# Optimization experiments

Measured on AMD Instinct MI355X. Metric: run time of the kernel, lower is better.

## Reference

```python
import jax, jax.numpy as jnp
import numpy as np

D_MODEL = 1024
N_HEADS = 16
HEAD_DIM = 64  # 16*64 = 1024
LATENT = 256   # low-rank KV compression dim
NUM_WHEELS = 4
WHEEL_OUT = 256


def setup_inputs() -> dict:
    key = jax.random.key(0)
    ks = jax.random.split(key, 9)
    S = 2048
    s = lambda fan_in: 1.0 / np.sqrt(fan_in)
    return {
        "sketch_emb": jax.random.normal(ks[0], (S, D_MODEL), dtype=jnp.float32),
        "Wq": jax.random.normal(ks[1], (D_MODEL, N_HEADS * HEAD_DIM), dtype=jnp.float32) * s(D_MODEL),
        "Wdkv": jax.random.normal(ks[2], (D_MODEL, LATENT), dtype=jnp.float32) * s(D_MODEL),
        "Wuk": jax.random.normal(ks[3], (LATENT, N_HEADS * HEAD_DIM), dtype=jnp.float32) * s(LATENT),
        "Wuv": jax.random.normal(ks[4], (LATENT, N_HEADS * HEAD_DIM), dtype=jnp.float32) * s(LATENT),
        "Wo": jax.random.normal(ks[5], (N_HEADS * HEAD_DIM, D_MODEL), dtype=jnp.float32) * s(N_HEADS * HEAD_DIM),
        "wheel_W": jax.random.normal(ks[6], (NUM_WHEELS, D_MODEL, WHEEL_OUT), dtype=jnp.float32) * s(D_MODEL),
        "wheel_b": jax.random.normal(ks[7], (NUM_WHEELS, WHEEL_OUT), dtype=jnp.float32) * 0.01,
    }


def reference(sketch_emb, Wq, Wdkv, Wuk, Wuv, Wo, wheel_W, wheel_b):
    S = sketch_emb.shape[0]
    # Multi-head latent attention: per-head Q, shared low-rank KV latent.
    q = (sketch_emb @ Wq).reshape(S, N_HEADS, HEAD_DIM)          # [S,H,D]
    c_kv = sketch_emb @ Wdkv                                      # [S,L]
    k = (c_kv @ Wuk).reshape(S, N_HEADS, HEAD_DIM)                # [S,H,D]
    v = (c_kv @ Wuv).reshape(S, N_HEADS, HEAD_DIM)                # [S,H,D]
    scale = 1.0 / np.sqrt(HEAD_DIM).astype(np.float32)
    scores = jnp.einsum("qhd,khd->hqk", q, k) * scale             # [H,S,S]
    attn = jax.nn.softmax(scores, axis=-1)
    ctx = jnp.einsum("hqk,khd->qhd", attn, v).reshape(S, N_HEADS * HEAD_DIM)
    body = ctx @ Wo                                               # [S,1024]
    # Wheel projections batched as one einsum, then laid out as concat order
    # cat([body, w0, w1, w2, w3], dim=1)
    wheels = jnp.einsum("sd,wde->swe", body, wheel_W) + wheel_b   # [S,W,256]
    wheels = wheels.reshape(S, NUM_WHEELS * WHEEL_OUT)
    return jnp.concatenate([body, wheels], axis=1)                # [S,2048]
```

## Files before the change

kernel.cpp:

```cpp
#include <hip/hip_runtime.h>
#include <math.h>

#define S_LEN 2048
#define DMODEL 1024
#define NHEADS 16
#define HDIM 64
#define QPITCH 1280

typedef _Float16 f16x8 __attribute__((ext_vector_type(8)));
typedef _Float16 f16x4 __attribute__((ext_vector_type(4)));
typedef float    f32x4 __attribute__((ext_vector_type(4)));

__device__ __forceinline__ void gld_lds16(void* lds, const void* g) {
    __builtin_amdgcn_global_load_lds(
        (__attribute__((address_space(1))) void*)(g),
        (__attribute__((address_space(3))) void*)(lds), 16, 0, 0);
}

__device__ __forceinline__ void gemm_core(
    _Float16* sA, _Float16* sB,
    const _Float16* __restrict__ A, int lda,
    const _Float16* __restrict__ Bt, int ldb,
    int nkt,
    _Float16* __restrict__ Cb, int ldcb, int bmode,
    _Float16* __restrict__ Cb2, int ldcb2,
    int bx, int by)
{
    const int tid  = threadIdx.x;
    const int lane = tid & 63;
    const int w    = tid >> 6;
    const int quad = lane >> 4;
    const int c0   = lane & 15;
    const int m0 = by * 128;
    const int n0 = bx * 128;

    const int srow = lane >> 3;
    const int sc   = lane & 7;
    const _Float16* a_src[4]; const _Float16* b_src[4];
    int dstoff[4];
#pragma unroll
    for (int t = 0; t < 4; t++) {
        const int row = w * 32 + t * 8 + srow;
        const int c = sc ^ (row & 7);
        a_src[t] = A  + (size_t)(m0 + row) * lda + c * 8;
        b_src[t] = Bt + (size_t)(n0 + row) * ldb + c * 8;
        dstoff[t] = (w * 32 + t * 8) * 64;
    }

    const int mw = (w & 1) * 64;
    const int nw = (w >> 1) * 64;
    int arow[4], brow[4];
#pragma unroll
    for (int i = 0; i < 4; i++) {
        arow[i] = mw + i * 16 + c0;
        brow[i] = nw + i * 16 + c0;
    }

    f32x4 acc[4][4];
#pragma unroll
    for (int i = 0; i < 4; i++)
#pragma unroll
        for (int j = 0; j < 4; j++) acc[i][j] = (f32x4){0.f, 0.f, 0.f, 0.f};

    auto stage = [&](int buf) {
#pragma unroll
        for (int t = 0; t < 4; t++) {
            gld_lds16(&sA[buf * 8192 + dstoff[t]], a_src[t]); a_src[t] += 64;
            gld_lds16(&sB[buf * 8192 + dstoff[t]], b_src[t]); b_src[t] += 64;
        }
    };
    auto step = [&](int buf) {
#pragma unroll
        for (int ks = 0; ks < 2; ks++) {
            const int cb = ks * 4 + quad;
            f16x8 af[4], bfv[4];
#pragma unroll
            for (int i = 0; i < 4; i++)
                af[i] = *(const f16x8*)&sA[buf * 8192 + arow[i] * 64 + ((cb ^ (arow[i] & 7)) << 3)];
#pragma unroll
            for (int j = 0; j < 4; j++)
                bfv[j] = *(const f16x8*)&sB[buf * 8192 + brow[j] * 64 + ((cb ^ (brow[j] & 7)) << 3)];
#pragma unroll
            for (int i = 0; i < 4; i++)
#pragma unroll
                for (int j = 0; j < 4; j++)
                    acc[i][j] = __builtin_amdgcn_mfma_f32_16x16x32_f16(af[i], bfv[j], acc[i][j], 0, 0, 0);
        }
    };

    stage(0);
    for (int kt = 0; kt < nkt; kt += 2) {
        __syncthreads();
        stage(1);
        step(0);
        __syncthreads();
        if (kt + 2 < nkt) stage(0);
        step(1);
    }

#pragma unroll
    for (int i = 0; i < 4; i++) {
#pragma unroll
        for (int reg = 0; reg < 4; reg++) {
            const int m = m0 + mw + i * 16 + quad * 4 + reg;
#pragma unroll
            for (int j = 0; j < 4; j++) {
                const int n = n0 + nw + j * 16 + c0;
                _Float16 hv = (_Float16)acc[i][j][reg];
                if (bmode == 0) {
                    Cb[(size_t)m * ldcb + n] = hv;
                } else {
                    if (n < 1024) Cb[(size_t)m * ldcb + n] = hv;
                    else {
                        const int col = (m & ~63) | (((m & 15) << 2) | ((m >> 4) & 3));
                        Cb2[(size_t)(n - 1024) * ldcb2 + col] = hv;
                    }
                }
            }
        }
    }
}

__global__ __launch_bounds__(256) void gemm_qcwf(
    const _Float16* __restrict__ WcT, const _Float16* __restrict__ Wo_f16,
    _Float16* __restrict__ BtWheels,
    const _Float16* __restrict__ emb_f16, const _Float16* __restrict__ Wqc_t,
    _Float16* __restrict__ qc_f16)
{
    __shared__ _Float16 sA[2][8192];
    __shared__ _Float16 sB[2][8192];
    int b = blockIdx.x;
    if (b < 64) {
        gemm_core(&sA[0][0], &sB[0][0], WcT, 1024, Wo_f16, 1024, 16,
                  BtWheels, 1024, 0, nullptr, 0, b >> 3, b & 7);
    } else {
        b -= 64;
        gemm_core(&sA[0][0], &sB[0][0], emb_f16, 1024, Wqc_t, 1024, 16,
                  qc_f16, 1280, 0, nullptr, 0, b >> 4, b & 15);
    }
}

__global__ __launch_bounds__(256) void gemm_kv(
    const _Float16* __restrict__ qc_f16, const _Float16* __restrict__ Wukv_t,
    _Float16* __restrict__ k_f16, _Float16* __restrict__ vT_f16)
{
    __shared__ _Float16 sA[2][8192];
    __shared__ _Float16 sB[2][8192];
    const int b = blockIdx.x;
    gemm_core(&sA[0][0], &sB[0][0], qc_f16 + 1024, 1280, Wukv_t, 256, 4,
              k_f16, 1024, 4, vT_f16, 2048, b >> 4, b & 15);
}

__global__ __launch_bounds__(256) void gemm_fin64(
    const _Float16* __restrict__ A,
    const _Float16* __restrict__ Bt,
    float* __restrict__ out,
    const float* __restrict__ bias)
{
    __shared__ _Float16 sA[2][64 * 64];
    __shared__ _Float16 sB[2][128 * 64];

    const int tid  = threadIdx.x;
    const int lane = tid & 63;
    const int w    = tid >> 6;
    const int quad = lane >> 4;
    const int c0   = lane & 15;

    const int flat = blockIdx.x;
    const int xcd  = flat & 7;
    const int wi   = flat >> 3;
    const int by   = (xcd & 3) * 8 + (wi & 7);
    const int bx   = (xcd >> 2) * 8 + (wi >> 3);
    const int m0 = by * 64;
    const int n0 = bx * 128;

    const int srow = lane >> 3;
    const int sc   = lane & 7;
    const _Float16* a_src[2]; int a_dst[2];
#pragma unroll
    for (int t = 0; t < 2; t++) {
        const int row = t * 32 + w * 8 + srow;
        const int c = sc ^ (row & 7);
        a_src[t] = A + (size_t)(m0 + row) * 1024 + c * 8;
        a_dst[t] = (t * 32 + w * 8) * 64;
    }
    const _Float16* b_src[4]; int b_dst[4];
#pragma unroll
    for (int t = 0; t < 4; t++) {
        const int row = t * 32 + w * 8 + srow;
        const int c = sc ^ (row & 7);
        b_src[t] = Bt + (size_t)(n0 + row) * 1024 + c * 8;
        b_dst[t] = (t * 32 + w * 8) * 64;
    }

    const int mw = (w & 1) * 32;
    const int nw = (w >> 1) * 64;
    int arow[2], brow[4];
#pragma unroll
    for (int i = 0; i < 2; i++) arow[i] = mw + i * 16 + c0;
#pragma unroll
    for (int j = 0; j < 4; j++) brow[j] = nw + j * 16 + c0;

    f32x4 acc[2][4];
#pragma unroll
    for (int i = 0; i < 2; i++)
#pragma unroll
        for (int j = 0; j < 4; j++) acc[i][j] = (f32x4){0.f, 0.f, 0.f, 0.f};

    auto stage = [&](int buf) {
#pragma unroll
        for (int t = 0; t < 2; t++) { gld_lds16(&sA[buf][a_dst[t]], a_src[t]); a_src[t] += 64; }
#pragma unroll
        for (int t = 0; t < 4; t++) { gld_lds16(&sB[buf][b_dst[t]], b_src[t]); b_src[t] += 64; }
    };
    auto step = [&](int buf) {
#pragma unroll
        for (int ks = 0; ks < 2; ks++) {
            const int cb = ks * 4 + quad;
            f16x8 af[2], bfv[4];
#pragma unroll
            for (int i = 0; i < 2; i++)
                af[i] = *(const f16x8*)&sA[buf][arow[i] * 64 + ((cb ^ (arow[i] & 7)) << 3)];
#pragma unroll
            for (int j = 0; j < 4; j++)
                bfv[j] = *(const f16x8*)&sB[buf][brow[j] * 64 + ((cb ^ (brow[j] & 7)) << 3)];
#pragma unroll
            for (int i = 0; i < 2; i++)
#pragma unroll
                for (int j = 0; j < 4; j++)
                    acc[i][j] = __builtin_amdgcn_mfma_f32_16x16x32_f16(af[i], bfv[j], acc[i][j], 0, 0, 0);
        }
    };

    stage(0);
    for (int kt = 0; kt < 16; kt += 2) {
        __syncthreads();
        stage(1);
        step(0);
        __syncthreads();
        if (kt + 2 < 16) stage(0);
        step(1);
    }

    float bias_v[4];
#pragma unroll
    for (int j = 0; j < 4; j++) bias_v[j] = bias[n0 + nw + j * 16 + c0];
#pragma unroll
    for (int i = 0; i < 2; i++) {
#pragma unroll
        for (int reg = 0; reg < 4; reg++) {
            const int m = m0 + mw + i * 16 + quad * 4 + reg;
#pragma unroll
            for (int j = 0; j < 4; j++) {
                const int n = n0 + nw + j * 16 + c0;
                out[(size_t)m * 2048 + n] = acc[i][j][reg] + bias_v[j];
            }
        }
    }
}

#define PITCH 72
#define SOFT_M2 8.65617024533378f

__global__ __launch_bounds__(256) void attn_mfma_kernel(
    const _Float16* __restrict__ qs,
    const _Float16* __restrict__ kk,
    const _Float16* __restrict__ vT,
    float* __restrict__ Opart,
    float* __restrict__ lpart)
{
    __shared__ _Float16 Ks[2][64 * 64];
    __shared__ _Float16 Vt[2][64 * 64];
    __shared__ _Float16 Ps[4 * 32 * PITCH];

    const int flat = blockIdx.x;
    const int g  = flat & 31;
    const int qb = flat >> 5;
    const int h  = g & 15;
    const int kz = g >> 4;
    const int tid  = threadIdx.x;
    const int lane = tid & 63;
    const int w    = tid >> 6;
    const int quad = lane >> 4;
    const int c0   = lane & 15;

    f16x8 qfrag[2][2];
#pragma unroll
    for (int m = 0; m < 2; m++) {
        const _Float16* qrow = qs + (size_t)(qb * 128 + w * 32 + m * 16 + c0) * QPITCH + h * HDIM;
        qfrag[m][0] = *(const f16x8*)(qrow + quad * 8);
        qfrag[m][1] = *(const f16x8*)(qrow + 32 + quad * 8);
    }

    const int srow = lane >> 3;
    const int sc   = lane & 7;
    const _Float16* k_src[2]; const _Float16* v_src[2];
    int dstoff[2];
#pragma unroll
    for (int t = 0; t < 2; t++) {
        const int row = w * 16 + t * 8 + srow;
        const int c = sc ^ (row & 7);
        k_src[t] = kk + (size_t)(kz * 1024 + row) * DMODEL + h * HDIM + c * 8;
        v_src[t] = vT + (size_t)(h * HDIM + row) * S_LEN + kz * 1024 + c * 8;
        dstoff[t] = (w * 16 + t * 8) * 64;
    }

    f32x4 Ofrag[2][4];
#pragma unroll
    for (int m = 0; m < 2; m++)
#pragma unroll
        for (int nb = 0; nb < 4; nb++) Ofrag[m][nb] = (f32x4){0.f, 0.f, 0.f, 0.f};
    float l_r[2][4] = {{0.f, 0.f, 0.f, 0.f}, {0.f, 0.f, 0.f, 0.f}};

    _Float16* Pw = Ps + w * (32 * PITCH);

    auto stage = [&](int buf) {
#pragma unroll
        for (int t = 0; t < 2; t++) {
            gld_lds16(&Ks[buf][dstoff[t]], k_src[t]); k_src[t] += (size_t)64 * DMODEL;
            gld_lds16(&Vt[buf][dstoff[t]], v_src[t]); v_src[t] += 64;
        }
    };

    auto attn_step = [&](int buf) {
        f32x4 sfrag[2][4];
#pragma unroll
        for (int m = 0; m < 2; m++)
#pragma unroll
            for (int nb = 0; nb < 4; nb++) sfrag[m][nb] = (f32x4){0.f, 0.f, 0.f, 0.f};
        __builtin_amdgcn_s_setprio(1);
#pragma unroll
        for (int nb = 0; nb < 4; nb++) {
            const int n = nb * 16 + c0;
#pragma unroll
            for (int ks = 0; ks < 2; ks++) {
                const int cb = ks * 4 + quad;
                f16x8 kfr = *(const f16x8*)&Ks[buf][n * 64 + ((cb ^ (n & 7)) << 3)];
#pragma unroll
                for (int m = 0; m < 2; m++)
                    sfrag[m][nb] = __builtin_amdgcn_mfma_f32_16x16x32_f16(qfrag[m][ks], kfr, sfrag[m][nb], 0, 0, 0);
            }
        }
        __builtin_amdgcn_s_setprio(0);

#pragma unroll
        for (int m = 0; m < 2; m++)
#pragma unroll
            for (int reg = 0; reg < 4; reg++) {
                float p0 = __builtin_amdgcn_exp2f(sfrag[m][0][reg] - SOFT_M2);
                float p1 = __builtin_amdgcn_exp2f(sfrag[m][1][reg] - SOFT_M2);
                float p2 = __builtin_amdgcn_exp2f(sfrag[m][2][reg] - SOFT_M2);
                float p3 = __builtin_amdgcn_exp2f(sfrag[m][3][reg] - SOFT_M2);
                sfrag[m][0][reg] = p0; sfrag[m][1][reg] = p1;
                sfrag[m][2][reg] = p2; sfrag[m][3][reg] = p3;
                l_r[m][reg] += p0 + p1 + p2 + p3;
            }

#pragma unroll
        for (int m = 0; m < 2; m++)
#pragma unroll
            for (int reg = 0; reg < 4; reg++) {
                const int prow = m * 16 + quad * 4 + reg;
                f16x4 pv;
                pv[0] = (_Float16)sfrag[m][0][reg];
                pv[1] = (_Float16)sfrag[m][1][reg];
                pv[2] = (_Float16)sfrag[m][2][reg];
                pv[3] = (_Float16)sfrag[m][3][reg];
                *(f16x4*)&Pw[prow * PITCH + c0 * 4] = pv;
            }
        __asm__ __volatile__("s_waitcnt lgkmcnt(0)" ::: "memory");

        f16x8 pfrag[2][2];
#pragma unroll
        for (int m = 0; m < 2; m++)
#pragma unroll
            for (int ks = 0; ks < 2; ks++)
                pfrag[m][ks] = *(const f16x8*)&Pw[(m * 16 + c0) * PITCH + ks * 32 + quad * 8];

        __builtin_amdgcn_s_setprio(1);
#pragma unroll
        for (int nb = 0; nb < 4; nb++) {
            const int n = nb * 16 + c0;
#pragma unroll
            for (int ks = 0; ks < 2; ks++) {
                const int cb = ks * 4 + quad;
                f16x8 vf = *(const f16x8*)&Vt[buf][n * 64 + ((cb ^ (n & 7)) << 3)];
#pragma unroll
                for (int m = 0; m < 2; m++)
                    Ofrag[m][nb] = __builtin_amdgcn_mfma_f32_16x16x32_f16(pfrag[m][ks], vf, Ofrag[m][nb], 0, 0, 0);
            }
        }
        __builtin_amdgcn_s_setprio(0);
    };

    stage(0);
    for (int kt = 0; kt < 16; kt += 2) {
        __syncthreads();
        stage(1);
        attn_step(0);
        __syncthreads();
        if (kt + 2 < 16) stage(0);
        attn_step(1);
    }

#pragma unroll
    for (int m = 0; m < 2; m++) {
#pragma unroll
        for (int reg = 0; reg < 4; reg++) {
            const int row = qb * 128 + w * 32 + m * 16 + quad * 4 + reg;
            float rsum = l_r[m][reg];
#pragma unroll
            for (int mask = 1; mask < 16; mask <<= 1)
                rsum += __shfl_xor(rsum, mask, 64);
            if (c0 == 0) lpart[(size_t)(kz * 16 + h) * 2048 + row] = rsum;
            float* op = Opart + ((size_t)kz * 2048 + row) * 1024 + h * HDIM;
#pragma unroll
            for (int nb = 0; nb < 4; nb++)
                op[nb * 16 + c0] = Ofrag[m][nb][reg];
        }
    }
}

__global__ __launch_bounds__(256) void attn_combine_kernel(
    const float* __restrict__ Opart, const float* __restrict__ lpart,
    _Float16* __restrict__ ctx)
{
    const int i = blockIdx.x * 256 + threadIdx.x;
    const int row = i >> 8;
    const int c4  = (i & 255) * 4;
    const int h = c4 >> 6;
    const float l = lpart[(size_t)h * 2048 + row] + lpart[(size_t)(16 + h) * 2048 + row];
    const float inv = 1.0f / l;
    float4 o0 = ((const float4*)(Opart + (size_t)row * 1024))[c4 >> 2];
    float4 o1 = ((const float4*)(Opart + (size_t)(2048 + row) * 1024))[c4 >> 2];
    f16x4 v;
    v[0] = (_Float16)((o0.x + o1.x) * inv);
    v[1] = (_Float16)((o0.y + o1.y) * inv);
    v[2] = (_Float16)((o0.z + o1.z) * inv);
    v[3] = (_Float16)((o0.w + o1.w) * inv);
    *(f16x4*)(ctx + (size_t)row * 1024 + c4) = v;
}

__device__ __forceinline__ void xpose_seg(float (*tile)[33],
    const float* __restrict__ src, _Float16* __restrict__ dst,
    int C, int dpitch, float scale, int bx, int by, int nbase0)
{
    const int r0 = by * 32, c0 = bx * 32;
    const int tr = threadIdx.x >> 5, tc = threadIdx.x & 31;
#pragma unroll
    for (int i = 0; i < 4; i++)
        tile[tr + i * 8][tc] = src[(size_t)(r0 + tr + i * 8) * C + c0 + tc];
    __syncthreads();
    const int nr = threadIdx.x & 31;
    const int k0 = (threadIdx.x >> 5) * 4;
    f16x4 hv;
#pragma unroll
    for (int e = 0; e < 4; e++)
        hv[e] = (_Float16)(tile[k0 + e][nr] * scale);
    *(f16x4*)(dst + (size_t)(nbase0 + c0 + nr) * dpitch + (r0 + k0)) = hv;
}

__global__ __launch_bounds__(256) void megaprep_kernel(
    const float* __restrict__ emb, const float* __restrict__ Wq,
    const float* __restrict__ Wdkv, const float* __restrict__ Wuk,
    const float* __restrict__ Wuv, const float* __restrict__ Wo,
    const float* __restrict__ wheelW, const float* __restrict__ wheelB,
    _Float16* __restrict__ Wqc_t, _Float16* __restrict__ Wukv_t,
    _Float16* __restrict__ Bt_full, _Float16* __restrict__ WcT,
    _Float16* __restrict__ Wo_f16, _Float16* __restrict__ emb_f16,
    float* __restrict__ biasbuf)
{
    __shared__ float tile[32][33];
    int b = blockIdx.x;
    const int tid = threadIdx.x;

    if (b < 1024) { xpose_seg(tile, Wq, Wqc_t, 1024, 1024, 0.125f, b & 31, b >> 5, 0); return; }
    b -= 1024;
    if (b < 256)  { xpose_seg(tile, Wdkv, Wqc_t + 1048576, 256, 1024, 1.f, b & 7, b >> 3, 0); return; }
    b -= 256;
    if (b < 256)  { xpose_seg(tile, Wuk, Wukv_t, 1024, 256, 1.4426950408889634f, b & 31, b >> 5, 0); return; }
    b -= 256;
    if (b < 256)  { xpose_seg(tile, Wuv, Wukv_t + 262144, 1024, 256, 1.f, b & 31, b >> 5, 0); return; }
    b -= 256;
    if (b < 1024) { xpose_seg(tile, Wo, Bt_full, 1024, 1024, 1.f, b & 31, b >> 5, 0); return; }
    b -= 1024;
    if (b < 1024) {
        const int z = b >> 8, rem = b & 255;
        xpose_seg(tile, wheelW + (size_t)z * 262144, WcT, 256, 1024, 1.f,
                  rem & 7, rem >> 3, z * 256);
        return;
    }
    b -= 1024;
    if (b < 1024) {
        const int i = b * 256 + tid;
        float4 f = ((const float4*)Wo)[i];
        f16x4 v;
        v[0] = (_Float16)f.x; v[1] = (_Float16)f.y;
        v[2] = (_Float16)f.z; v[3] = (_Float16)f.w;
        ((f16x4*)Wo_f16)[i] = v;
        return;
    }
    b -= 1024;
    if (b < 2048) {
        const int i = b * 256 + tid;
        float4 f = ((const float4*)emb)[i];
        f16x4 v;
        v[0] = (_Float16)f.x; v[1] = (_Float16)f.y;
        v[2] = (_Float16)f.z; v[3] = (_Float16)f.w;
        ((f16x4*)emb_f16)[i] = v;
        return;
    }
    b -= 2048;
    if (b < 8) {
        const int i = b * 256 + tid;
        biasbuf[i] = (i < 1024) ? 0.f : wheelB[i - 1024];
    }
}

extern "C" void kernel_launch(void* const* d_in, const int* in_sizes, int n_in,
                              void* d_out, int out_size, void* d_ws, size_t ws_size,
                              hipStream_t stream) {
    const float* emb    = (const float*)d_in[0];
    const float* Wq     = (const float*)d_in[1];
    const float* Wdkv   = (const float*)d_in[2];
    const float* Wuk    = (const float*)d_in[3];
    const float* Wuv    = (const float*)d_in[4];
    const float* Wo     = (const float*)d_in[5];
    const float* wheelW = (const float*)d_in[6];
    const float* wheelB = (const float*)d_in[7];
    float* out = (float*)d_out;

    _Float16* ws = (_Float16*)d_ws;
    _Float16* Bt_full = ws;
    _Float16* Wqc_t   = ws + 2097152;
    _Float16* Wukv_t  = ws + 3407872;
    float*    biasbuf = (float*)(ws + 3932160);
    _Float16* WcT     = ws + 3936256;
    _Float16* Wo_f16  = ws + 4984832;
    _Float16* ctx     = ws + 3936256;
    _Float16* emb_f16 = ws + 6033408;
    _Float16* qc_f16  = ws + 8130560;
    _Float16* k_f16   = ws + 10752000;
    _Float16* vT_f16  = ws + 12849152;
    float*    Opart   = (float*)(ws + 14946304);
    float*    lpart   = (float*)(ws + 23334912);

    megaprep_kernel<<<6920, 256, 0, stream>>>(
        emb, Wq, Wdkv, Wuk, Wuv, Wo, wheelW, wheelB,
        Wqc_t, Wukv_t, Bt_full, WcT, Wo_f16, emb_f16, biasbuf);

    gemm_qcwf<<<224, 256, 0, stream>>>(WcT, Wo_f16, Bt_full + (size_t)1024 * 1024,
                                       emb_f16, Wqc_t, qc_f16);

    gemm_kv<<<256, 256, 0, stream>>>(qc_f16, Wukv_t, k_f16, vT_f16);

    attn_mfma_kernel<<<512, 256, 0, stream>>>(qc_f16, k_f16, vT_f16, Opart, lpart);

    attn_combine_kernel<<<2048, 256, 0, stream>>>(Opart, lpart, ctx);

    gemm_fin64<<<512, 256, 0, stream>>>(ctx, Bt_full, out, biasbuf);
}
```

Baseline: 171.4 us.

## Keep softmax probabilities in registers via transposed MFMA in attention

```diff
diff --git a/kernel.cpp b/kernel.cpp
--- a/kernel.cpp
+++ b/kernel.cpp
@@ -111,10 +111,7 @@
                     Cb[(size_t)m * ldcb + n] = hv;
                 } else {
                     if (n < 1024) Cb[(size_t)m * ldcb + n] = hv;
-                    else {
-                        const int col = (m & ~63) | (((m & 15) << 2) | ((m >> 4) & 3));
-                        Cb2[(size_t)(n - 1024) * ldcb2 + col] = hv;
-                    }
+                    else          Cb2[(size_t)(n - 1024) * ldcb2 + m] = hv;
                 }
             }
         }
@@ -259,8 +256,8 @@
     }
 }
 
-#define PITCH 72
 #define SOFT_M2 8.65617024533378f
+#define OTP 68
 
 __global__ __launch_bounds__(256) void attn_mfma_kernel(
     const _Float16* __restrict__ qs,
@@ -271,7 +268,7 @@
 {
     __shared__ _Float16 Ks[2][64 * 64];
     __shared__ _Float16 Vt[2][64 * 64];
-    __shared__ _Float16 Ps[4 * 32 * PITCH];
+    __shared__ float    Ot[4][16 * OTP];
 
     const int flat = blockIdx.x;
     const int g  = flat & 31;
@@ -305,14 +302,12 @@
         dstoff[t] = (w * 16 + t * 8) * 64;
     }
 
-    f32x4 Ofrag[2][4];
+    f32x4 OfragT[2][4];
 #pragma unroll
     for (int m = 0; m < 2; m++)
 #pragma unroll
-        for (int nb = 0; nb < 4; nb++) Ofrag[m][nb] = (f32x4){0.f, 0.f, 0.f, 0.f};
-    float l_r[2][4] = {{0.f, 0.f, 0.f, 0.f}, {0.f, 0.f, 0.f, 0.f}};
-
-    _Float16* Pw = Ps + w * (32 * PITCH);
+        for (int db = 0; db < 4; db++) OfragT[m][db] = (f32x4){0.f, 0.f, 0.f, 0.f};
+    float l_r[2] = {0.f, 0.f};
 
     auto stage = [&](int buf) {
 #pragma unroll
@@ -331,63 +326,44 @@
         __builtin_amdgcn_s_setprio(1);
 #pragma unroll
         for (int nb = 0; nb < 4; nb++) {
-            const int n = nb * 16 + c0;
+            const int krow = nb * 16 + c0;
 #pragma unroll
             for (int ks = 0; ks < 2; ks++) {
                 const int cb = ks * 4 + quad;
-                f16x8 kfr = *(const f16x8*)&Ks[buf][n * 64 + ((cb ^ (n & 7)) << 3)];
+                f16x8 kfr = *(const f16x8*)&Ks[buf][krow * 64 + ((cb ^ (c0 & 7)) << 3)];
 #pragma unroll
                 for (int m = 0; m < 2; m++)
-                    sfrag[m][nb] = __builtin_amdgcn_mfma_f32_16x16x32_f16(qfrag[m][ks], kfr, sfrag[m][nb], 0, 0, 0);
+                    sfrag[m][nb] = __builtin_amdgcn_mfma_f32_16x16x32_f16(kfr, qfrag[m][ks], sfrag[m][nb], 0, 0, 0);
             }
         }
         __builtin_amdgcn_s_setprio(0);
 
+        f16x4 pfrag[2][4];
 #pragma unroll
         for (int m = 0; m < 2; m++)
 #pragma unroll
-            for (int reg = 0; reg < 4; reg++) {
-                float p0 = __builtin_amdgcn_exp2f(sfrag[m][0][reg] - SOFT_M2);
-                float p1 = __builtin_amdgcn_exp2f(sfrag[m][1][reg] - SOFT_M2);
-                float p2 = __builtin_amdgcn_exp2f(sfrag[m][2][reg] - SOFT_M2);
-                float p3 = __builtin_amdgcn_exp2f(sfrag[m][3][reg] - SOFT_M2);
-                sfrag[m][0][reg] = p0; sfrag[m][1][reg] = p1;
-                sfrag[m][2][reg] = p2; sfrag[m][3][reg] = p3;
-                l_r[m][reg] += p0 + p1 + p2 + p3;
+            for (int kb = 0; kb < 4; kb++) {
+                float p0 = __builtin_amdgcn_exp2f(sfrag[m][kb][0] - SOFT_M2);
+                float p1 = __builtin_amdgcn_exp2f(sfrag[m][kb][1] - SOFT_M2);
+                float p2 = __builtin_amdgcn_exp2f(sfrag[m][kb][2] - SOFT_M2);
+                float p3 = __builtin_amdgcn_exp2f(sfrag[m][kb][3] - SOFT_M2);
+                l_r[m] += (p0 + p1) + (p2 + p3);
+                f16x4 pv;
+                pv[0] = (_Float16)p0; pv[1] = (_Float16)p1;
+                pv[2] = (_Float16)p2; pv[3] = (_Float16)p3;
+                pfrag[m][kb] = pv;
             }
 
-#pragma unroll
-        for (int m = 0; m < 2; m++)
-#pragma unroll
-            for (int reg = 0; reg < 4; reg++) {
-                const int prow = m * 16 + quad * 4 + reg;
-                f16x4 pv;
-                pv[0] = (_Float16)sfrag[m][0][reg];
-                pv[1] = (_Float16)sfrag[m][1][reg];
-                pv[2] = (_Float16)sfrag[m][2][reg];
-                pv[3] = (_Float16)sfrag[m][3][reg];
-                *(f16x4*)&Pw[prow * PITCH + c0 * 4] = pv;
-            }
-        __asm__ __volatile__("s_waitcnt lgkmcnt(0)" ::: "memory");
-
-        f16x8 pfrag[2][2];
-#pragma unroll
-        for (int m = 0; m < 2; m++)
-#pragma unroll
-            for (int ks = 0; ks < 2; ks++)
-                pfrag[m][ks] = *(const f16x8*)&Pw[(m * 16 + c0) * PITCH + ks * 32 + quad * 8];
-
         __builtin_amdgcn_s_setprio(1);
 #pragma unroll
-        for (int nb = 0; nb < 4; nb++) {
-            const int n = nb * 16 + c0;
-#pragma unroll
-            for (int ks = 0; ks < 2; ks++) {
-                const int cb = ks * 4 + quad;
-                f16x8 vf = *(const f16x8*)&Vt[buf][n * 64 + ((cb ^ (n & 7)) << 3)];
+        for (int kb = 0; kb < 4; kb++) {
+            const int cc = (((kb * 2 + (quad >> 1)) ^ (c0 & 7)) << 3) + (quad & 1) * 4;
+#pragma unroll
+            for (int db = 0; db < 4; db++) {
+                f16x4 vf = *(const f16x4*)&Vt[buf][(db * 16 + c0) * 64 + cc];
 #pragma unroll
                 for (int m = 0; m < 2; m++)
-                    Ofrag[m][nb] = __builtin_amdgcn_mfma_f32_16x16x32_f16(pfrag[m][ks], vf, Ofrag[m][nb], 0, 0, 0);
+                    OfragT[m][db] = __builtin_amdgcn_mfma_f32_16x16x16f16(vf, pfrag[m][kb], OfragT[m][db], 0, 0, 0);
             }
         }
         __builtin_amdgcn_s_setprio(0);
@@ -405,19 +381,28 @@
 
 #pragma unroll
     for (int m = 0; m < 2; m++) {
-#pragma unroll
-        for (int reg = 0; reg < 4; reg++) {
-            const int row = qb * 128 + w * 32 + m * 16 + quad * 4 + reg;
-            float rsum = l_r[m][reg];
-#pragma unroll
-            for (int mask = 1; mask < 16; mask <<= 1)
-                rsum += __shfl_xor(rsum, mask, 64);
-            if (c0 == 0) lpart[(size_t)(kz * 16 + h) * 2048 + row] = rsum;
-            float* op = Opart + ((size_t)kz * 2048 + row) * 1024 + h * HDIM;
-#pragma unroll
-            for (int nb = 0; nb < 4; nb++)
-                op[nb * 16 + c0] = Ofrag[m][nb][reg];
-        }
+        float rs = l_r[m];
+        rs += __shfl_xor(rs, 16, 64);
+        rs += __shfl_xor(rs, 32, 64);
+        if (lane < 16)
+            lpart[(size_t)(kz * 16 + h) * 2048 + qb * 128 + w * 32 + m * 16 + c0] = rs;
+    }
+
+    float* Otw = &Ot[w][0];
+#pragma unroll
+    for (int m = 0; m < 2; m++) {
+#pragma unroll
+        for (int db = 0; db < 4; db++)
+            *(f32x4*)&Otw[c0 * OTP + db * 16 + quad * 4] = OfragT[m][db];
+        __asm__ __volatile__("s_waitcnt lgkmcnt(0)" ::: "memory");
+#pragma unroll
+        for (int it = 0; it < 4; it++) {
+            const int r = it * 4 + quad;
+            f32x4 ov = *(const f32x4*)&Otw[r * OTP + c0 * 4];
+            const int row = qb * 128 + w * 32 + m * 16 + r;
+            *(f32x4*)&Opart[((size_t)kz * 2048 + row) * 1024 + h * 64 + c0 * 4] = ov;
+        }
+        __asm__ __volatile__("s_waitcnt lgkmcnt(0)" ::: "memory");
     }
 }
 
```

After: 170.9 us. About the same (-0.3%).
